# Optimization experiments

Measured on AMD Instinct MI355X. Metric: run time of the kernel, lower is better.

Reference implementation:

```python
import jax, jax.numpy as jnp
import numpy as np

N_NODES = 100000
N_EDGES = 1600000
IN_DIM = 128
HID = 128
N_CLASSES = 16
N_GRAPHS = 512


def setup_inputs() -> dict:
    key = jax.random.key(0)
    ks = jax.random.split(key, 16)
    d = {
        "x": jax.random.normal(ks[0], (N_NODES, IN_DIM), jnp.float32),
        "src": jax.random.randint(ks[1], (N_EDGES,), 0, N_NODES, jnp.int64 if jax.config.jax_enable_x64 else jnp.int32),
        "dst": jax.random.randint(ks[2], (N_EDGES,), 0, N_NODES, jnp.int64 if jax.config.jax_enable_x64 else jnp.int32),
        "gid": jnp.sort(jax.random.randint(ks[3], (N_NODES,), 0, N_GRAPHS, jnp.int64 if jax.config.jax_enable_x64 else jnp.int32)),
    }
    s = 1.0 / np.sqrt(HID)
    for i, k in zip(range(1, 5), ks[4:8]):
        d[f"W{i}"] = jax.random.uniform(k, (HID, HID), jnp.float32, -s, s)
        d[f"b{i}"] = jnp.zeros((HID,), jnp.float32)
    d["Wv"] = jax.random.uniform(ks[8], (HID, 1), jnp.float32, -s, s)
    d["bv"] = jnp.zeros((1,), jnp.float32)
    d["Wc"] = jax.random.uniform(ks[9], (HID, N_CLASSES), jnp.float32, -s, s)
    d["bc"] = jnp.zeros((N_CLASSES,), jnp.float32)
    return d


def _gcn_layer(h, W, b, src, dst, norm_src, norm_dst):
    # DGL GraphConv, norm='both': D_dst^{-1/2} * A * D_src^{-1/2} * h * W + b, then ReLU outside
    m = (h * norm_src[:, None])[src]                                  # [E, H] edge gather
    agg = jax.ops.segment_sum(m, dst, num_segments=N_NODES)           # [N, H] scatter-add
    return jax.nn.relu(agg * norm_dst[:, None] @ W + b)


def reference(x, W1, b1, W2, b2, W3, b3, W4, b4, Wv, bv, Wc, bc, src, dst, gid):
    ones = jnp.ones((N_EDGES,), jnp.float32)
    deg_out = jnp.clip(jax.ops.segment_sum(ones, src, num_segments=N_NODES), 1.0)
    deg_in = jnp.clip(jax.ops.segment_sum(ones, dst, num_segments=N_NODES), 1.0)
    norm_src = jax.lax.rsqrt(deg_out)
    norm_dst = jax.lax.rsqrt(deg_in)

    h = _gcn_layer(x, W1, b1, src, dst, norm_src, norm_dst)
    h = _gcn_layer(h, W2, b2, src, dst, norm_src, norm_dst)
    h = _gcn_layer(h, W3, b3, src, dst, norm_src, norm_dst)
    h = _gcn_layer(h, W4, b4, src, dst, norm_src, norm_dst)

    w = jax.nn.sigmoid(h @ Wv + bv)                                   # [N, 1]
    num = jax.ops.segment_sum(h * w, gid, num_segments=N_GRAPHS)      # [G, H]
    den = jax.ops.segment_sum(w, gid, num_segments=N_GRAPHS)          # [G, 1]
    hg = jnp.where(den > 0, num / jnp.where(den > 0, den, 1.0), 0.0)  # weighted mean readout
    return hg @ Wc + bc                                               # [G, n_classes]
```

## Files before the change

kernel.cpp:

```cpp
#include <hip/hip_runtime.h>
#include <hip/hip_bf16.h>

#define N_NODES_C 100000
#define N_EDGES_C 1600000
#define HID_C 128
#define NCLS_C 16
#define NGRAPH_C 512
#define SCAN_BLK 1024
#define NCHUNK ((N_NODES_C + SCAN_BLK - 1) / SCAN_BLK)
#define FILL_PASSES 4
#define FILL_RANGE ((N_NODES_C + FILL_PASSES - 1) / FILL_PASSES)

__global__ void k_count_src(const int* __restrict__ src, int* cnt_out) {
  int i = blockIdx.x * blockDim.x + threadIdx.x;
  if (i < N_EDGES_C / 4) {
    int4 v = ((const int4*)src)[i];
    atomicAdd(&cnt_out[v.x], 1);
    atomicAdd(&cnt_out[v.y], 1);
    atomicAdd(&cnt_out[v.z], 1);
    atomicAdd(&cnt_out[v.w], 1);
  }
}

__global__ void k_count_dst(const int* __restrict__ dst, int* cnt_in) {
  int i = blockIdx.x * blockDim.x + threadIdx.x;
  if (i < N_EDGES_C / 4) {
    int4 v = ((const int4*)dst)[i];
    atomicAdd(&cnt_in[v.x], 1);
    atomicAdd(&cnt_in[v.y], 1);
    atomicAdd(&cnt_in[v.z], 1);
    atomicAdd(&cnt_in[v.w], 1);
  }
}

__global__ void k_norm(const int* __restrict__ cnt_out, const int* __restrict__ cnt_in,
                       float* norm_src, float* norm_dst) {
  int i = blockIdx.x * blockDim.x + threadIdx.x;
  if (i < N_NODES_C) {
    norm_src[i] = 1.f / sqrtf(fmaxf((float)cnt_out[i], 1.f));
    norm_dst[i] = 1.f / sqrtf(fmaxf((float)cnt_in[i], 1.f));
  }
}

__global__ void k_scan1(const int* __restrict__ cnt, int* part) {
  __shared__ int s[SCAN_BLK];
  int tid = threadIdx.x;
  int i = blockIdx.x * SCAN_BLK + tid;
  s[tid] = (i < N_NODES_C) ? cnt[i] : 0;
  __syncthreads();
  for (int off = SCAN_BLK / 2; off > 0; off >>= 1) {
    if (tid < off) s[tid] += s[tid + off];
    __syncthreads();
  }
  if (tid == 0) part[blockIdx.x] = s[0];
}

__global__ void k_scan2(int* part, int* row_start) {
  if (threadIdx.x == 0 && blockIdx.x == 0) {
    int run = 0;
    for (int i = 0; i < NCHUNK; ++i) { int v = part[i]; part[i] = run; run += v; }
    row_start[N_NODES_C] = run;
  }
}

__global__ void k_scan3(const int* __restrict__ cnt, const int* __restrict__ part,
                        int* row_start, int* cursor) {
  __shared__ int s[SCAN_BLK];
  int tid = threadIdx.x;
  int i = blockIdx.x * SCAN_BLK + tid;
  int x = (i < N_NODES_C) ? cnt[i] : 0;
  s[tid] = x;
  __syncthreads();
  for (int off = 1; off < SCAN_BLK; off <<= 1) {
    int v = (tid >= off) ? s[tid - off] : 0;
    __syncthreads();
    s[tid] += v;
    __syncthreads();
  }
  if (i < N_NODES_C) {
    int excl = part[blockIdx.x] + s[tid] - x;
    row_start[i] = excl;
    cursor[i] = excl;
  }
}

__global__ void k_fill(const int* __restrict__ src, const int* __restrict__ dst,
                       int* cursor, int* __restrict__ csr_src) {
  int tid0 = blockIdx.x * blockDim.x + threadIdx.x;
  int stride = gridDim.x * blockDim.x;
#pragma unroll 1
  for (int pass = 0; pass < FILL_PASSES; ++pass) {
    int lo = pass * FILL_RANGE;
    int hi = lo + FILL_RANGE;
    for (int i = tid0; i < N_EDGES_C; i += stride) {
      int d = dst[i];
      if (d >= lo && d < hi) {
        int p = atomicAdd(&cursor[d], 1);
        csr_src[p] = src[i];
      }
    }
  }
}

__global__ void k_gstart(const int* __restrict__ gid, int* __restrict__ gstart) {
  int n = blockIdx.x * blockDim.x + threadIdx.x;
  if (n >= N_NODES_C) return;
  int g = gid[n];
  int gp = (n == 0) ? -1 : gid[n - 1];
  for (int k = gp + 1; k <= g; ++k) gstart[k] = n;
  if (n == N_NODES_C - 1) {
    for (int k = g + 1; k <= NGRAPH_C; ++k) gstart[k] = N_NODES_C;
  }
}

__device__ __forceinline__ int swz_col(int n) {
  return (n < 64) ? n : 64 + ((n - 60) & 63);
}

__global__ __launch_bounds__(256) void k_gemm_rowscale(
    const float* __restrict__ A, const float* __restrict__ W,
    const float* __restrict__ rowscale, float* __restrict__ T, int rows) {
  __shared__ float sA[64][132];
  __shared__ float sB[64][128];
  int t = threadIdx.x;
  int tx = t & 15, ty = t >> 4;
  int m0 = blockIdx.x * 128;

  float acc[8][8];
#pragma unroll
  for (int i = 0; i < 8; ++i)
#pragma unroll
    for (int j = 0; j < 8; ++j) acc[i][j] = 0.f;

  int a_c4 = (t & 15) * 4;
  int a_r = t >> 4;
  int w_n4 = (t & 31) * 4;
  int w_k = t >> 5;
  int w_ns = swz_col(w_n4);

  int b0 = swz_col(tx * 8);
  int b1 = swz_col(tx * 8 + 4);

  for (int k0 = 0; k0 < HID_C; k0 += 64) {
#pragma unroll
    for (int rr = 0; rr < 8; ++rr) {
      int r = rr * 16 + a_r;
      int row = m0 + r;
      float4 v = make_float4(0.f, 0.f, 0.f, 0.f);
      if (row < rows) v = *(const float4*)&A[(size_t)row * HID_C + k0 + a_c4];
      sA[a_c4 + 0][r] = v.x;
      sA[a_c4 + 1][r] = v.y;
      sA[a_c4 + 2][r] = v.z;
      sA[a_c4 + 3][r] = v.w;
    }
#pragma unroll
    for (int i = 0; i < 8; ++i) {
      int kc = i * 8 + w_k;
      float4 v = *(const float4*)&W[(size_t)(k0 + kc) * HID_C + w_n4];
      *(float4*)&sB[kc][w_ns] = v;
    }
    __syncthreads();

#pragma unroll 2
    for (int kk = 0; kk < 64; ++kk) {
      float4 a0 = *(const float4*)&sA[kk][ty * 8];
      float4 a1 = *(const float4*)&sA[kk][ty * 8 + 4];
      float4 bb0 = *(const float4*)&sB[kk][b0];
      float4 bb1 = *(const float4*)&sB[kk][b1];
      float a[8] = {a0.x, a0.y, a0.z, a0.w, a1.x, a1.y, a1.z, a1.w};
      float b[8] = {bb0.x, bb0.y, bb0.z, bb0.w, bb1.x, bb1.y, bb1.z, bb1.w};
#pragma unroll
      for (int i = 0; i < 8; ++i)
#pragma unroll
        for (int j = 0; j < 8; ++j) acc[i][j] = fmaf(a[i], b[j], acc[i][j]);
    }
    __syncthreads();
  }

#pragma unroll
  for (int i = 0; i < 8; ++i) {
    int row = m0 + ty * 8 + i;
    if (row < rows) {
      float sc = rowscale[row];
      float4 v0 = {acc[i][0] * sc, acc[i][1] * sc, acc[i][2] * sc, acc[i][3] * sc};
      float4 v1 = {acc[i][4] * sc, acc[i][5] * sc, acc[i][6] * sc, acc[i][7] * sc};
      float4* p = (float4*)&T[(size_t)row * HID_C + tx * 8];
      p[0] = v0;
      p[1] = v1;
    }
  }
}

__global__ __launch_bounds__(256) void k_agg(
    const float* __restrict__ T, const int* __restrict__ row_start,
    const int* __restrict__ csr_src, const float* __restrict__ norm_dst,
    const float* __restrict__ bias, float* __restrict__ H) {
  int wid = threadIdx.x >> 6, lane = threadIdx.x & 63;
  int n = blockIdx.x * 4 + wid;
  if (n >= N_NODES_C) return;
  int s0 = row_start[n], s1 = row_start[n + 1];
  const float2* T2 = (const float2*)T;
  float ax = 0.f, ay = 0.f;
  int e = s0;
  for (; e + 8 <= s1; e += 8) {
    int a0 = csr_src[e + 0], a1 = csr_src[e + 1];
    int a2 = csr_src[e + 2], a3 = csr_src[e + 3];
    int a4 = csr_src[e + 4], a5 = csr_src[e + 5];
    int a6 = csr_src[e + 6], a7 = csr_src[e + 7];
    float2 v0 = T2[(size_t)a0 * 64 + lane];
    float2 v1 = T2[(size_t)a1 * 64 + lane];
    float2 v2 = T2[(size_t)a2 * 64 + lane];
    float2 v3 = T2[(size_t)a3 * 64 + lane];
    float2 v4 = T2[(size_t)a4 * 64 + lane];
    float2 v5 = T2[(size_t)a5 * 64 + lane];
    float2 v6 = T2[(size_t)a6 * 64 + lane];
    float2 v7 = T2[(size_t)a7 * 64 + lane];
    ax += v0.x + v1.x + v2.x + v3.x + v4.x + v5.x + v6.x + v7.x;
    ay += v0.y + v1.y + v2.y + v3.y + v4.y + v5.y + v6.y + v7.y;
  }
  for (; e < s1; ++e) {
    int a = csr_src[e];
    float2 v = T2[(size_t)a * 64 + lane];
    ax += v.x;
    ay += v.y;
  }
  float nd = norm_dst[n];
  float bx = bias[2 * lane], by = bias[2 * lane + 1];
  float2 r;
  r.x = fmaxf(fmaf(ax, nd, bx), 0.f);
  r.y = fmaxf(fmaf(ay, nd, by), 0.f);
  ((float2*)H)[(size_t)n * 64 + lane] = r;
}

__global__ __launch_bounds__(256) void k_readout(
    const float* __restrict__ H, const float* __restrict__ Wv,
    const float* __restrict__ bv, const int* __restrict__ gstart,
    const float* __restrict__ Wc, const float* __restrict__ bc,
    float* __restrict__ out) {
  int g = blockIdx.x;
  int wid = threadIdx.x >> 6, lane = threadIdx.x & 63;
  int s0 = gstart[g], s1 = gstart[g + 1];
  float2 wv2 = ((const float2*)Wv)[lane];
  float bvs = bv[0];
  float ax = 0.f, ay = 0.f, dw = 0.f;
  for (int n = s0 + wid; n < s1; n += 4) {
    float2 h2 = ((const float2*)H)[(size_t)n * 64 + lane];
    float p = h2.x * wv2.x + h2.y * wv2.y;
#pragma unroll
    for (int off = 32; off > 0; off >>= 1) p += __shfl_xor(p, off);
    float w = 1.f / (1.f + expf(-(p + bvs)));
    ax += h2.x * w;
    ay += h2.y * w;
    dw += w;
  }
  __shared__ float2 snum[4][64];
  __shared__ float sden[4];
  __shared__ float hg[HID_C];
  snum[wid][lane] = make_float2(ax, ay);
  if (lane == 0) sden[wid] = dw;
  __syncthreads();
  if (wid == 0) {
    float2 a = snum[0][lane], b = snum[1][lane], c = snum[2][lane], d = snum[3][lane];
    float den = sden[0] + sden[1] + sden[2] + sden[3];
    float inv = (den > 0.f) ? 1.f / den : 0.f;
    hg[2 * lane] = (a.x + b.x + c.x + d.x) * inv;
    hg[2 * lane + 1] = (a.y + b.y + c.y + d.y) * inv;
  }
  __syncthreads();
  if (threadIdx.x < NCLS_C) {
    int c = threadIdx.x;
    float acc = 0.f;
    for (int k = 0; k < HID_C; ++k) acc = fmaf(hg[k], Wc[k * NCLS_C + c], acc);
    out[g * NCLS_C + c] = acc + bc[c];
  }
}

extern "C" void kernel_launch(void* const* d_in, const int* in_sizes, int n_in,
                              void* d_out, int out_size, void* d_ws, size_t ws_size,
                              hipStream_t stream) {
  const float* x = (const float*)d_in[0];
  const int* src = (const int*)d_in[1];
  const int* dst = (const int*)d_in[2];
  const int* gid = (const int*)d_in[3];
  const float* W[4] = {(const float*)d_in[4], (const float*)d_in[6],
                       (const float*)d_in[8], (const float*)d_in[10]};
  const float* b[4] = {(const float*)d_in[5], (const float*)d_in[7],
                       (const float*)d_in[9], (const float*)d_in[11]};
  const float* Wv = (const float*)d_in[12];
  const float* bv = (const float*)d_in[13];
  const float* Wc = (const float*)d_in[14];
  const float* bc = (const float*)d_in[15];
  float* out = (float*)d_out;

  char* ws = (char*)d_ws;
  size_t off = 0;
  auto alloc = [&](size_t bytes) -> char* {
    char* p = ws + off;
    off = (off + bytes + 255) & ~(size_t)255;
    return p;
  };
  int* cnt_out = (int*)alloc((size_t)N_NODES_C * 4);
  int* cnt_in = (int*)alloc((size_t)N_NODES_C * 4);
  float* norm_src = (float*)alloc((size_t)N_NODES_C * 4);
  float* norm_dst = (float*)alloc((size_t)N_NODES_C * 4);
  int* row_start = (int*)alloc((size_t)(N_NODES_C + 1) * 4);
  int* cursor = (int*)alloc((size_t)N_NODES_C * 4);
  int* part = (int*)alloc((size_t)SCAN_BLK * 4);
  int* gstart = (int*)alloc((size_t)(NGRAPH_C + 1) * 4);
  int* csr_src = (int*)alloc((size_t)N_EDGES_C * 4);
  float* tbuf = (float*)alloc((size_t)N_NODES_C * HID_C * 4);
  float* hbuf = (float*)alloc((size_t)N_NODES_C * HID_C * 4);
  (void)ws_size;
  (void)in_sizes;
  (void)n_in;
  (void)out_size;

  hipMemsetAsync(cnt_out, 0, (size_t)N_NODES_C * 4, stream);
  hipMemsetAsync(cnt_in, 0, (size_t)N_NODES_C * 4, stream);

  int count_grid = (N_EDGES_C / 4 + 255) / 256;
  k_count_src<<<count_grid, 256, 0, stream>>>(src, cnt_out);
  k_count_dst<<<count_grid, 256, 0, stream>>>(dst, cnt_in);
  k_norm<<<(N_NODES_C + 255) / 256, 256, 0, stream>>>(cnt_out, cnt_in, norm_src, norm_dst);
  k_scan1<<<NCHUNK, SCAN_BLK, 0, stream>>>(cnt_in, part);
  k_scan2<<<1, 1, 0, stream>>>(part, row_start);
  k_scan3<<<NCHUNK, SCAN_BLK, 0, stream>>>(cnt_in, part, row_start, cursor);
  k_fill<<<2048, 256, 0, stream>>>(src, dst, cursor, csr_src);
  k_gstart<<<(N_NODES_C + 255) / 256, 256, 0, stream>>>(gid, gstart);

  int gemm_grid = (N_NODES_C + 127) / 128;
  int node_grid = (N_NODES_C + 3) / 4;
  const float* hin = x;
  for (int l = 0; l < 4; ++l) {
    k_gemm_rowscale<<<gemm_grid, 256, 0, stream>>>(hin, W[l], norm_src, tbuf, N_NODES_C);
    k_agg<<<node_grid, 256, 0, stream>>>(tbuf, row_start, csr_src, norm_dst, b[l], hbuf);
    hin = hbuf;
  }

  k_readout<<<NGRAPH_C, 256, 0, stream>>>(hbuf, Wv, bv, gstart, Wc, bc, out);
}
```

Measured before the change: 968.8 us.

## Store GEMM output in feature-sliced layout and aggregate per slice

The GEMM now writes its output as 16 feature slices of 8 floats per node, so each slice of the transformed features (3.2 MB) can stay cache-resident while the aggregation kernel gathers from it. The aggregation is rewritten so blocks are mapped to (slice, 64-node chunk), with 8 lanes per edge and 8 edges in flight per wavefront, followed by a shuffle reduction. The GEMM K-tile is also halved to 32 and the column swizzle is removed. In exchange, each node's CSR index list is read 16 times and each gather fetches only 32 bytes per edge, and the plain column indexing may reintroduce LDS bank conflicts.

```diff
diff --git a/kernel.cpp b/kernel.cpp
--- a/kernel.cpp
+++ b/kernel.cpp
@@ -10,6 +10,10 @@
 #define NCHUNK ((N_NODES_C + SCAN_BLK - 1) / SCAN_BLK)
 #define FILL_PASSES 4
 #define FILL_RANGE ((N_NODES_C + FILL_PASSES - 1) / FILL_PASSES)
+#define NSLICE 16
+#define SLICE_STRIDE ((size_t)N_NODES_C * 8)
+#define AGG_NODES 64
+#define NCHUNK_T ((N_NODES_C + AGG_NODES - 1) / AGG_NODES)
 
 __global__ void k_count_src(const int* __restrict__ src, int* cnt_out) {
   int i = blockIdx.x * blockDim.x + threadIdx.x;
@@ -113,15 +117,11 @@
   }
 }
 
-__device__ __forceinline__ int swz_col(int n) {
-  return (n < 64) ? n : 64 + ((n - 60) & 63);
-}
-
 __global__ __launch_bounds__(256) void k_gemm_rowscale(
     const float* __restrict__ A, const float* __restrict__ W,
     const float* __restrict__ rowscale, float* __restrict__ T, int rows) {
-  __shared__ float sA[64][132];
-  __shared__ float sB[64][128];
+  __shared__ float sA[32][132];
+  __shared__ float sB[32][132];
   int t = threadIdx.x;
   int tx = t & 15, ty = t >> 4;
   int m0 = blockIdx.x * 128;
@@ -132,19 +132,15 @@
 #pragma unroll
     for (int j = 0; j < 8; ++j) acc[i][j] = 0.f;
 
-  int a_c4 = (t & 15) * 4;
-  int a_r = t >> 4;
+  int a_c4 = (t & 7) * 4;
+  int a_r = t >> 3;
   int w_n4 = (t & 31) * 4;
   int w_k = t >> 5;
-  int w_ns = swz_col(w_n4);
-
-  int b0 = swz_col(tx * 8);
-  int b1 = swz_col(tx * 8 + 4);
-
-  for (int k0 = 0; k0 < HID_C; k0 += 64) {
-#pragma unroll
-    for (int rr = 0; rr < 8; ++rr) {
-      int r = rr * 16 + a_r;
+
+  for (int k0 = 0; k0 < HID_C; k0 += 32) {
+#pragma unroll
+    for (int rr = 0; rr < 4; ++rr) {
+      int r = rr * 32 + a_r;
       int row = m0 + r;
       float4 v = make_float4(0.f, 0.f, 0.f, 0.f);
       if (row < rows) v = *(const float4*)&A[(size_t)row * HID_C + k0 + a_c4];
@@ -154,19 +150,19 @@
       sA[a_c4 + 3][r] = v.w;
     }
 #pragma unroll
-    for (int i = 0; i < 8; ++i) {
+    for (int i = 0; i < 4; ++i) {
       int kc = i * 8 + w_k;
       float4 v = *(const float4*)&W[(size_t)(k0 + kc) * HID_C + w_n4];
-      *(float4*)&sB[kc][w_ns] = v;
-    }
-    __syncthreads();
-
-#pragma unroll 2
-    for (int kk = 0; kk < 64; ++kk) {
+      *(float4*)&sB[kc][w_n4] = v;
+    }
+    __syncthreads();
+
+#pragma unroll 4
+    for (int kk = 0; kk < 32; ++kk) {
       float4 a0 = *(const float4*)&sA[kk][ty * 8];
       float4 a1 = *(const float4*)&sA[kk][ty * 8 + 4];
-      float4 bb0 = *(const float4*)&sB[kk][b0];
-      float4 bb1 = *(const float4*)&sB[kk][b1];
+      float4 bb0 = *(const float4*)&sB[kk][tx * 8];
+      float4 bb1 = *(const float4*)&sB[kk][tx * 8 + 4];
       float a[8] = {a0.x, a0.y, a0.z, a0.w, a1.x, a1.y, a1.z, a1.w};
       float b[8] = {bb0.x, bb0.y, bb0.z, bb0.w, bb1.x, bb1.y, bb1.z, bb1.w};
 #pragma unroll
@@ -177,6 +173,7 @@
     __syncthreads();
   }
 
+  float* Ts = T + (size_t)tx * SLICE_STRIDE;
 #pragma unroll
   for (int i = 0; i < 8; ++i) {
     int row = m0 + ty * 8 + i;
@@ -184,52 +181,58 @@
       float sc = rowscale[row];
       float4 v0 = {acc[i][0] * sc, acc[i][1] * sc, acc[i][2] * sc, acc[i][3] * sc};
       float4 v1 = {acc[i][4] * sc, acc[i][5] * sc, acc[i][6] * sc, acc[i][7] * sc};
-      float4* p = (float4*)&T[(size_t)row * HID_C + tx * 8];
+      float4* p = (float4*)&Ts[(size_t)row * 8];
       p[0] = v0;
       p[1] = v1;
     }
   }
 }
 
-__global__ __launch_bounds__(256) void k_agg(
+__global__ __launch_bounds__(256) void k_agg_t(
     const float* __restrict__ T, const int* __restrict__ row_start,
     const int* __restrict__ csr_src, const float* __restrict__ norm_dst,
     const float* __restrict__ bias, float* __restrict__ H) {
+  int bid = blockIdx.x;
+  int s_lo = bid & 7;
+  int q = bid >> 3;
+  int s_hi = q / NCHUNK_T;
+  int chunk = q - s_hi * NCHUNK_T;
+  int s = s_hi * 8 + s_lo;
+
   int wid = threadIdx.x >> 6, lane = threadIdx.x & 63;
-  int n = blockIdx.x * 4 + wid;
-  if (n >= N_NODES_C) return;
-  int s0 = row_start[n], s1 = row_start[n + 1];
-  const float2* T2 = (const float2*)T;
-  float ax = 0.f, ay = 0.f;
-  int e = s0;
-  for (; e + 8 <= s1; e += 8) {
-    int a0 = csr_src[e + 0], a1 = csr_src[e + 1];
-    int a2 = csr_src[e + 2], a3 = csr_src[e + 3];
-    int a4 = csr_src[e + 4], a5 = csr_src[e + 5];
-    int a6 = csr_src[e + 6], a7 = csr_src[e + 7];
-    float2 v0 = T2[(size_t)a0 * 64 + lane];
-    float2 v1 = T2[(size_t)a1 * 64 + lane];
-    float2 v2 = T2[(size_t)a2 * 64 + lane];
-    float2 v3 = T2[(size_t)a3 * 64 + lane];
-    float2 v4 = T2[(size_t)a4 * 64 + lane];
-    float2 v5 = T2[(size_t)a5 * 64 + lane];
-    float2 v6 = T2[(size_t)a6 * 64 + lane];
-    float2 v7 = T2[(size_t)a7 * 64 + lane];
-    ax += v0.x + v1.x + v2.x + v3.x + v4.x + v5.x + v6.x + v7.x;
-    ay += v0.y + v1.y + v2.y + v3.y + v4.y + v5.y + v6.y + v7.y;
-  }
-  for (; e < s1; ++e) {
-    int a = csr_src[e];
-    float2 v = T2[(size_t)a * 64 + lane];
-    ax += v.x;
-    ay += v.y;
-  }
-  float nd = norm_dst[n];
-  float bx = bias[2 * lane], by = bias[2 * lane + 1];
-  float2 r;
-  r.x = fmaxf(fmaf(ax, nd, bx), 0.f);
-  r.y = fmaxf(fmaf(ay, nd, by), 0.f);
-  ((float2*)H)[(size_t)n * 64 + lane] = r;
+  int j = lane >> 3;
+  int f = lane & 7;
+  const float* Ts = T + (size_t)s * SLICE_STRIDE;
+  float bvf = bias[s * 8 + f];
+
+  int n0 = chunk * AGG_NODES + wid * 16;
+#pragma unroll 1
+  for (int nn = 0; nn < 16; ++nn) {
+    int n = n0 + nn;
+    if (n >= N_NODES_C) break;
+    int s0 = row_start[n], s1 = row_start[n + 1];
+    float acc0 = 0.f, acc1 = 0.f;
+    for (int e0 = s0; e0 < s1; e0 += 16) {
+      int ea = e0 + j;
+      int eb = e0 + 8 + j;
+      int ca = ea < s1 ? ea : s1 - 1;
+      int cb = eb < s1 ? eb : s1 - 1;
+      int ia = __builtin_nontemporal_load(&csr_src[ca]);
+      int ib = __builtin_nontemporal_load(&csr_src[cb]);
+      float va = Ts[(size_t)ia * 8 + f];
+      float vb = Ts[(size_t)ib * 8 + f];
+      acc0 += (ea < s1) ? va : 0.f;
+      acc1 += (eb < s1) ? vb : 0.f;
+    }
+    float acc = acc0 + acc1;
+    acc += __shfl_xor(acc, 8);
+    acc += __shfl_xor(acc, 16);
+    acc += __shfl_xor(acc, 32);
+    if (lane < 8) {
+      float nd = norm_dst[n];
+      H[(size_t)n * HID_C + s * 8 + f] = fmaxf(fmaf(acc, nd, bvf), 0.f);
+    }
+  }
 }
 
 __global__ __launch_bounds__(256) void k_readout(
@@ -329,11 +332,11 @@
   k_gstart<<<(N_NODES_C + 255) / 256, 256, 0, stream>>>(gid, gstart);
 
   int gemm_grid = (N_NODES_C + 127) / 128;
-  int node_grid = (N_NODES_C + 3) / 4;
+  int agg_grid = NSLICE * NCHUNK_T;
   const float* hin = x;
   for (int l = 0; l < 4; ++l) {
     k_gemm_rowscale<<<gemm_grid, 256, 0, stream>>>(hin, W[l], norm_src, tbuf, N_NODES_C);
-    k_agg<<<node_grid, 256, 0, stream>>>(tbuf, row_start, csr_src, norm_dst, b[l], hbuf);
+    k_agg_t<<<agg_grid, 256, 0, stream>>>(tbuf, row_start, csr_src, norm_dst, b[l], hbuf);
     hin = hbuf;
   }
 
```

Measured after the change: 2.465 ms. 2.54x slower.
